# Optimization experiments

Hardware: AMD Instinct MI355X
Metric: run time of the kernel (lower is better)

The kernel has to match this reference:

```python
import jax, jax.numpy as jnp
import numpy as np

V, D, H, B, S, T, N_EXTRA = 32000, 256, 512, 16, 400, 100, 50


def _lstm_cell(x, h, c, Wih, Whh, b):
    g = x @ Wih.T + h @ Whh.T + b
    i, f, gg, o = jnp.split(g, 4, axis=-1)
    c = jax.nn.sigmoid(f) * c + jax.nn.sigmoid(i) * jnp.tanh(gg)
    h = jax.nn.sigmoid(o) * jnp.tanh(c)
    return h, c


def _run_lstm(xs, m, Wih, Whh, b):
    # xs: [S,B,D], m: [S,B,1] validity mask (packed-sequence semantics)
    Bz, Hh = xs.shape[1], Whh.shape[1]
    init = (jnp.zeros((Bz, Hh), xs.dtype), jnp.zeros((Bz, Hh), xs.dtype))
    def step(carry, inp):
        h, c = carry
        x, mm = inp
        hn, cn = _lstm_cell(x, h, c, Wih, Whh, b)
        h = jnp.where(mm, hn, h)
        c = jnp.where(mm, cn, c)
        return (h, c), jnp.where(mm, hn, 0.0)
    (h, c), ys = jax.lax.scan(step, init, (xs, m))
    return ys, h, c


def setup_inputs():
    key = jax.random.key(0)
    ks = jax.random.split(key, 20)
    def gn(k, shape, scale=0.05):
        return jax.random.normal(k, shape, dtype=jnp.float32) * scale
    inp = {}
    inp["source"] = jax.random.randint(ks[0], (B, S), 0, V)
    inp["source_extended"] = jax.random.randint(ks[1], (B, S), 0, V + N_EXTRA)
    inp["source_length"] = jax.random.randint(ks[2], (B,), S // 2, S + 1)
    inp["target"] = jax.random.randint(ks[3], (B, T), 0, V)
    inp["emb"] = gn(ks[4], (V, D), 0.1)
    inp["enc_Wih_f"] = gn(ks[5], (4 * H, D))
    inp["enc_Whh_f"] = gn(ks[6], (4 * H, H))
    inp["enc_b_f"] = jnp.zeros((4 * H,), jnp.float32)
    inp["enc_Wih_b"] = gn(ks[7], (4 * H, D))
    inp["enc_Whh_b"] = gn(ks[8], (4 * H, H))
    inp["enc_b_b"] = jnp.zeros((4 * H,), jnp.float32)
    inp["Wproj"] = gn(ks[9], (H, 2 * H))
    inp["bproj"] = jnp.zeros((H,), jnp.float32)
    inp["W2h"] = gn(ks[10], (H, 2 * H))
    inp["b2h"] = jnp.zeros((H,), jnp.float32)
    inp["W2c"] = gn(ks[11], (H, 2 * H))
    inp["b2c"] = jnp.zeros((H,), jnp.float32)
    inp["Wo1"] = gn(ks[12], (H, 2 * H))
    inp["bo1"] = jnp.zeros((H,), jnp.float32)
    inp["Wo2"] = gn(ks[13], (D, H))
    inp["dec_Wih"] = gn(ks[14], (4 * H, 2 * D))
    inp["dec_Whh"] = gn(ks[15], (4 * H, H))
    inp["dec_b"] = jnp.zeros((4 * H,), jnp.float32)
    inp["Wpgen"] = gn(ks[16], (1, 2 * H + 2 * D))
    inp["bpgen"] = jnp.zeros((1,), jnp.float32)
    return inp


def reference(source, source_extended, source_length, target, emb,
              enc_Wih_f, enc_Whh_f, enc_b_f, enc_Wih_b, enc_Whh_b, enc_b_b,
              Wproj, bproj, W2h, b2h, W2c, b2c, Wo1, bo1, Wo2,
              dec_Wih, dec_Whh, dec_b, Wpgen, bpgen):
    mask = jnp.arange(S)[None, :] < source_length[:, None]  # [B,S]
    w_s = emb[source]                                        # [B,S,D]
    xs = jnp.swapaxes(w_s, 0, 1)                             # [S,B,D]
    m = jnp.swapaxes(mask, 0, 1)[:, :, None]                 # [S,B,1]
    # bidirectional LSTM encoder
    ys_f, h_f, c_f = _run_lstm(xs, m, enc_Wih_f, enc_Whh_f, enc_b_f)
    ys_b, h_b, c_b = _run_lstm(xs[::-1], m[::-1], enc_Wih_b, enc_Whh_b, enc_b_b)
    ys_b = ys_b[::-1]
    enc_outs = jnp.swapaxes(jnp.concatenate([ys_f, ys_b], -1), 0, 1)  # [B,S,2H]
    enc_outs = enc_outs @ Wproj.T + bproj                             # [B,S,H]
    dec_h = jnp.concatenate([h_f, h_b], -1) @ W2h.T + b2h             # [B,H]
    dec_c = jnp.concatenate([c_f, c_b], -1) @ W2c.T + b2c             # [B,H]
    lens = source_length[:, None].astype(enc_outs.dtype)
    seq_mean = (enc_outs * mask[..., None]).sum(1) / lens             # [B,H]
    def out_proj(x):
        return jnp.tanh(x @ Wo1.T + bo1) @ Wo2.T
    dec_out0 = out_proj(jnp.concatenate([dec_h, seq_mean], -1))       # [B,D]
    neg = jnp.finfo(enc_outs.dtype).min
    extra = jnp.zeros((B, N_EXTRA), enc_outs.dtype)
    rows = jnp.arange(B)[:, None]
    w_t = jnp.swapaxes(emb[target], 0, 1)                             # [T,B,D]
    def step(carry, x_t):
        dec_out, h, c = carry
        x = jnp.concatenate([x_t, dec_out], -1)                       # [B,2D]
        h, c = _lstm_cell(x, h, c, dec_Wih, dec_Whh, dec_b)
        scores = jnp.einsum('bh,bsh->bs', h, enc_outs)
        attn = jax.nn.softmax(jnp.where(mask, scores, neg), axis=-1)  # point_dist
        context = jnp.einsum('bs,bsh->bh', attn, enc_outs)
        p_gen = jax.nn.sigmoid(jnp.concatenate([context, h, x], -1) @ Wpgen.T + bpgen)  # [B,1]
        dec_out = out_proj(jnp.concatenate([h, context], -1))         # [B,D]
        logit = dec_out @ emb.T                                       # [B,V]
        vocab_dist = jnp.concatenate([p_gen * jax.nn.softmax(logit, axis=-1), extra], -1)
        final = vocab_dist.at[rows, source_extended].add((1.0 - p_gen) * attn) + 1e-20
        return (dec_out, h, c), jnp.log(final)
    _, logits = jax.lax.scan(step, (dec_out0, dec_h, dec_c), w_t)
    return logits  # [T,B,V+N_EXTRA]
```

## Files before the change

kernel.cpp:

```cpp
#include <hip/hip_runtime.h>

#define V_SZ 32000
#define D_SZ 256
#define H_SZ 512
#define B_SZ 16
#define S_SZ 400
#define T_SZ 100
#define G4   2048
#define VX   32050
#define LINE 32

typedef unsigned short ushort_t;
typedef __attribute__((ext_vector_type(8))) __bf16 bf16x8;
typedef __attribute__((ext_vector_type(8))) unsigned short ushort8_t;
typedef __attribute__((ext_vector_type(4))) float f32x4;

__device__ __forceinline__ ushort_t f2bf(float x) {
  union { float f; unsigned u; } v; v.f = x;
  unsigned r = v.u + 0x7fffu + ((v.u >> 16) & 1u);
  return (ushort_t)(r >> 16);
}
__device__ __forceinline__ float bf2f(ushort_t x) {
  union { unsigned u; float f; } v; v.u = ((unsigned)x) << 16; return v.f;
}
__device__ __forceinline__ float bfu2f(unsigned x) {
  union { unsigned u; float f; } v; v.u = x << 16; return v.f;
}
__device__ __forceinline__ float sigf(float x) { return 1.0f / (1.0f + __expf(-x)); }
__device__ __forceinline__ float tanh_f(float x) {
  float e = __expf(2.0f * x);
  return 1.0f - 2.0f / (e + 1.0f);
}
__device__ __forceinline__ float dot4(f32x4 a, f32x4 b) {
  return a.x * b.x + a.y * b.y + a.z * b.z + a.w * b.w;
}
__device__ __forceinline__ void stg(float* p, float v) {
  __hip_atomic_store(p, v, __ATOMIC_RELAXED, __HIP_MEMORY_SCOPE_AGENT);
}
__device__ __forceinline__ void stg_u32(unsigned* p, unsigned v) {
  __hip_atomic_store(p, v, __ATOMIC_RELAXED, __HIP_MEMORY_SCOPE_AGENT);
}
__device__ __forceinline__ unsigned pollu(const unsigned* p) {
  return __hip_atomic_load(p, __ATOMIC_RELAXED, __HIP_MEMORY_SCOPE_AGENT);
}
__device__ __forceinline__ unsigned ld_sc0(const unsigned* p) {
  unsigned v;
  asm volatile("global_load_dword %0, %1, off sc0\n\ts_waitcnt vmcnt(0)"
               : "=&v"(v) : "v"(p) : "memory");
  return v;
}
__device__ __forceinline__ int xcc_id() {
  unsigned v;
  asm volatile("s_getreg_b32 %0, hwreg(HW_REG_XCC_ID)" : "=s"(v));
  return (int)(v & 0xf);
}

__device__ __forceinline__ void slot_barrier(unsigned* slots, int myslot, int nslots,
                                             unsigned pc) {
  asm volatile("s_waitcnt vmcnt(0)" ::: "memory");
  __syncthreads();
  if (threadIdx.x == 0)
    __hip_atomic_store(&slots[myslot * LINE], pc, __ATOMIC_RELAXED, __HIP_MEMORY_SCOPE_AGENT);
  if (threadIdx.x < 64) {
    const int i0 = threadIdx.x, i1 = threadIdx.x + 64;
    for (;;) {
      unsigned v0 = pc, v1 = pc;
      if (i0 < nslots)
        v0 = __hip_atomic_load(&slots[i0 * LINE], __ATOMIC_RELAXED, __HIP_MEMORY_SCOPE_AGENT);
      if (i1 < nslots)
        v1 = __hip_atomic_load(&slots[i1 * LINE], __ATOMIC_RELAXED, __HIP_MEMORY_SCOPE_AGENT);
      if (__all((v0 >= pc) & (v1 >= pc))) break;
      __builtin_amdgcn_s_sleep(1);
    }
  }
  __syncthreads();
}

__global__ __launch_bounds__(256) void cvt_kernel(const float* in, ushort_t* outp, int n) {
  int i = blockIdx.x * 256 + threadIdx.x;
  int stride = gridDim.x * 256;
  for (; i < n; i += stride) outp[i] = f2bf(in[i]);
}

__global__ __launch_bounds__(256) void cvt_strided_kernel(const float* in, ushort_t* outp) {
  int gid = blockIdx.x * 256 + threadIdx.x;
  int r = gid >> 8, d = gid & 255;
  outp[gid] = f2bf(in[(size_t)r * 512 + d]);
}

__global__ __launch_bounds__(256) void cvt_wo2t_kernel(const float* wo2, ushort_t* outp) {
  int gid = blockIdx.x * 256 + threadIdx.x;
  int h = gid >> 8, d = gid & 255;
  outp[gid] = f2bf(wo2[(size_t)d * 512 + h]);
}

__global__ __launch_bounds__(256) void wfused_kernel(const float* dwih, const float* wo2,
                                                     float* wf) {
  __shared__ float xr_s[256];
  int r = blockIdx.x;
  xr_s[threadIdx.x] = dwih[(size_t)r * 512 + 256 + threadIdx.x];
  __syncthreads();
  float a0 = 0, a1 = 0;
  for (int d = 0; d < 256; ++d) {
    float x = xr_s[d];
    a0 += x * wo2[(size_t)d * 512 + threadIdx.x];
    a1 += x * wo2[(size_t)d * 512 + threadIdx.x + 256];
  }
  wf[(size_t)r * 512 + threadIdx.x] = a0;
  wf[(size_t)r * 512 + threadIdx.x + 256] = a1;
}

__global__ __launch_bounds__(256) void wfp_kernel(const float* wpgen, const float* wo2,
                                                  float* wfp) {
  int h = blockIdx.x * 256 + threadIdx.x;
  float a = 0;
  for (int d = 0; d < 256; ++d) a += wpgen[1280 + d] * wo2[(size_t)d * 512 + h];
  wfp[h] = a;
}

__global__ __launch_bounds__(256) void pack_whh_kernel(const float* whh_f, const float* whh_b,
                                                       ushort_t* outp) {
  int gid = blockIdx.x * 256 + threadIdx.x;
  int col = gid & 511;
  int p_g = gid >> 9;
  int dir = p_g >> 11, p = p_g & 2047;
  int ub = p >> 6, g = (p >> 4) & 3, u = p & 15;
  const float* src = dir ? whh_b : whh_f;
  outp[gid] = f2bf(src[(size_t)(g * 512 + ub * 16 + u) * 512 + col]);
// ... 94 lines not shown
      int m = m0 + kh * 4 + i;
      int b = m & 15, si = m >> 4;
      enc_outs[((size_t)b * S_SZ + si) * H_SZ + n] = acc[s][i] + bv;
    }
  }
}

__global__ __launch_bounds__(256) void gemm_e2(const ushort_t* emb_bf, const ushort_t* wo2t_bf,
                                               ushort_t* e2) {
  int wave = threadIdx.x >> 6;
  int m0 = blockIdx.y * 16;
  int n0 = blockIdx.x * 256 + wave * 64;
  f32x4 acc[4] = {};
  mfma_16x64(emb_bf, wo2t_bf, 256, m0, n0, acc);
  int lane = threadIdx.x & 63, lr = lane & 15, kh = lane >> 4;
#pragma unroll
  for (int s = 0; s < 4; ++s) {
    int n = n0 + s * 16 + lr;
#pragma unroll
    for (int i = 0; i < 4; ++i) {
      int m = m0 + kh * 4 + i;
      e2[(size_t)m * 512 + n] = f2bf(acc[s][i]);
    }
  }
}

__global__ __launch_bounds__(256) void gemm_logits(const ushort_t* tmp_bf, const ushort_t* e2_bf,
                                                   float* out) {
  int wave = threadIdx.x >> 6;
  int m0 = blockIdx.x * 16;
  int n0 = blockIdx.y * 256 + wave * 64;
  f32x4 acc[4] = {};
  mfma_16x64(tmp_bf, e2_bf, 512, m0, n0, acc);
  int lane = threadIdx.x & 63, lr = lane & 15, kh = lane >> 4;
#pragma unroll
  for (int s = 0; s < 4; ++s) {
    int n = n0 + s * 16 + lr;
#pragma unroll
    for (int i = 0; i < 4; ++i) {
      int m = m0 + kh * 4 + i;
      out[(size_t)m * VX + n] = acc[s][i];
    }
  }
}

__global__ __launch_bounds__(256, 1) void enc_kernel(const float* gx_f, const float* gx_b,
                                                     const ushort_t* whh_pk, const int* src_len,
                                                     unsigned* hb_f, unsigned* hb_b,
                                                     unsigned* hbM_f, unsigned* hbM_b,
                                                     unsigned* ys_cat_u32, float* h_final,
                                                     float* c_final, unsigned* ctrs) {
  __shared__ float big_s[25600];
  __shared__ int role_s;
  __shared__ int ok_s;
  float* gates_s = big_s;
  const int tid = threadIdx.x;
  if (tid == 0) {
    int xcc = xcc_id();
    int r = -1;
    if (xcc == 0) {
      unsigned i = atomicAdd(&ctrs[12288], 1u);
      if (i < 32u) r = (int)i;
    } else if (xcc == 1) {
      unsigned i = atomicAdd(&ctrs[12320], 1u);
      if (i < 32u) r = 32 + (int)i;
    }
    role_s = r;
  }
  __syncthreads();
  const int role = role_s;
  if (role < 0) return;
  const int dir = role >> 5, ub = role & 31, j0 = ub * 16;
  const int g = tid >> 6, lane = tid & 63, lr = lane & 15, kh = lane >> 4;
  const float* gx = dir ? gx_b : gx_f;
  unsigned* hb = dir ? hb_b : hb_f;
  unsigned* hbM = dir ? hbM_b : hbM_f;
  unsigned* tl = ctrs + dir * 1024;
  unsigned* tm = ctrs + 2048 + dir * 1024;
  const ushort_t* wrow =
      whh_pk + (size_t)(((dir * 32 + ub) * 4 + g) * 16 + lr) * 512 + kh * 8;
  const int bc = tid >> 4, uc = tid & 15;
  const int len_b = src_len[bc];
  float c_reg = 0.0f, h_reg = 0.0f;
  bool slow = false;

  int maxlen;
  {
    int v = src_len[lane & 15];
    v = max(v, __shfl_xor(v, 1));
    v = max(v, __shfl_xor(v, 2));
    v = max(v, __shfl_xor(v, 4));
    v = max(v, __shfl_xor(v, 8));
    maxlen = v;
  }
  for (int i = tid; i < (S_SZ - maxlen) * 128; i += 256) {
    int s = maxlen + (i >> 7);
    int r2 = i & 127;
    int bb = r2 >> 3, k = r2 & 7;
    ys_cat_u32[(size_t)(s * 16 + bb) * 512 + dir * 256 + (j0 >> 1) + k] = 0u;
  }

  float gxa[4];
  {
    const int s0 = dir ? (maxlen - 1) : 0;
    const float* g0 = gx + (size_t)s0 * (16 * 2048) + g * 512 + j0 + lr;
#pragma unroll
    for (int i = 0; i < 4; ++i) gxa[i] = g0[(size_t)(kh * 4 + i) * 2048];
  }

  for (int t = 0; t < maxlen; ++t) {
    const int s_pos = dir ? (maxlen - 1 - t) : t;
    float gxn[4] = {0.f, 0.f, 0.f, 0.f};
    if (t + 1 < maxlen) {
      const int sn = dir ? (maxlen - 2 - t) : (t + 1);
      const float* gn = gx + (size_t)sn * (16 * 2048) + g * 512 + j0 + lr;
#pragma unroll
      for (int i = 0; i < 4; ++i) gxn[i] = gn[(size_t)(kh * 4 + i) * 2048];
    }
    const unsigned* hsrcbuf = hb;
    if (t > 0) {
      if (tid < 64) {
        int ok = 0;
        if (!slow) {
          for (int it = 0; it < 2000; ++it) {
            unsigned v = (unsigned)t;
            if (lane < 32) v = ld_sc0(&tl[lane * 32]);
            if (__all((int)(v >= (unsigned)t))) { ok = 1; break; }
            __builtin_amdgcn_s_sleep(1);
          }
        }
        if (!ok) {
          for (;;) {
            unsigned v = (unsigned)t;
            if (lane < 32) v = pollu(&tm[lane * 32]);
            if (__all((int)(v >= (unsigned)t))) break;
            __builtin_amdgcn_s_sleep(1);
          }
        }
        if (tid == 0) ok_s = ok;
      }
      __syncthreads();
      if (!ok_s) slow = true;
      hsrcbuf = ok_s ? hb : hbM;
    }
    f32x4 acc = {0.f, 0.f, 0.f, 0.f};
    const ushort_t* ap = (const ushort_t*)(hsrcbuf + (size_t)t * 4096) + lr * 512 + kh * 8;
#pragma unroll
    for (int k0 = 0; k0 < 512; k0 += 32)
      acc = __builtin_amdgcn_mfma_f32_16x16x32_bf16(*(const bf16x8*)(ap + k0),
                                                    *(const bf16x8*)(wrow + k0), acc, 0, 0, 0);
#pragma unroll
    for (int i = 0; i < 4; ++i)
      gates_s[(g * 16 + lr) * 17 + kh * 4 + i] = acc[i] + gxa[i];
    __syncthreads();
    float gi = gates_s[uc * 17 + bc];
    float gf = gates_s[(16 + uc) * 17 + bc];
    float gg = gates_s[(32 + uc) * 17 + bc];
    float go = gates_s[(48 + uc) * 17 + bc];
    bool msk = s_pos < len_b;
    float cn = sigf(gf) * c_reg + sigf(gi) * tanh_f(gg);
    float hn = sigf(go) * tanh_f(cn);
    float hout = msk ? hn : h_reg;
    if (msk) c_reg = cn;
    h_reg = hout;
    unsigned hbits = (unsigned)f2bf(hout);
    unsigned hpart = __shfl_xor(hbits, 1);
    unsigned ybits = msk ? (unsigned)f2bf(hn) : 0u;
    unsigned ypart = __shfl_xor(ybits, 1);
    if ((uc & 1) == 0) {
      unsigned wv2 = hbits | (hpart << 16);
      size_t ix = (size_t)(t + 1) * 4096 + bc * 256 + ((j0 + uc) >> 1);
      hb[ix] = wv2;
      stg_u32(&hbM[ix], wv2);
      ys_cat_u32[(size_t)(s_pos * 16 + bc) * 512 + dir * 256 + ((j0 + uc) >> 1)] =
          ybits | (ypart << 16);
    }
    if (t == maxlen - 1) {
      h_final[dir * 8192 + bc * 512 + j0 + uc] = hout;
      c_final[dir * 8192 + bc * 512 + j0 + uc] = c_reg;
    }
    asm volatile("s_waitcnt vmcnt(0)" ::: "memory");
    __syncthreads();
    if (tid == 0) {
      tl[ub * 32] = (unsigned)(t + 1);
      stg_u32(&tm[ub * 32], (unsigned)(t + 1));
    }
#pragma unroll
    for (int i = 0; i < 4; ++i) gxa[i] = gxn[i];
  }
}

__global__ __launch_bounds__(256) void seqmean_kernel(const float* enc_outs, const int* src_len,
                                                      float* seq_mean) {
  int b = blockIdx.x >> 1;
  int j = (blockIdx.x & 1) * 256 + threadIdx.x;
  int L = src_len[b];
  float a = 0;
  for (int s = 0; s < L; ++s) a += enc_outs[((size_t)b * S_SZ + s) * H_SZ + j];
  seq_mean[b * 512 + j] = a / (float)L;
}

__global__ __launch_bounds__(256) void init_state_kernel(const float* h_final, const float* c_final,
                                                         const float* w2h, const float* b2h,
                                                         const float* w2c, const float* b2c,
                                                         unsigned* h_u32, float* c_init) {
  int gid = blockIdx.x * 256 + threadIdx.x;
  int half = gid >> 13;
  int idx = gid & 8191;
  int b = idx >> 9, j = idx & 511;
  const float* src = half ? c_final : h_final;
  const float* w = (half ? w2c : w2h) + (size_t)j * 1024;
  float acc = (half ? b2c : b2h)[j];
  const f32x4* s0 = (const f32x4*)(src + b * 512);
  const f32x4* s1 = (const f32x4*)(src + 8192 + b * 512);
  const f32x4* w0 = (const f32x4*)w;
  const f32x4* w1 = w0 + 128;
  float a = 0;
  for (int k = 0; k < 128; ++k) a += dot4(s0[k], w0[k]);
  for (int k = 0; k < 128; ++k) a += dot4(s1[k], w1[k]);
  acc += a;
  if (half) {
    c_init[idx] = acc;
  } else {
    unsigned bits = (unsigned)f2bf(acc);
    unsigned pb2 = __shfl_xor(bits, 1);
    if ((j & 1) == 0) h_u32[b * 256 + (j >> 1)] = bits | (pb2 << 16);
  }
}

__global__ __launch_bounds__(256) void tmp0_kernel(const unsigned* h0_u32, const float* seq_mean,
                                                   const float* wo1, const float* bo1,
                                                   unsigned* tmp_u32) {
  int gid = blockIdx.x * 256 + threadIdx.x;
  int b = gid >> 9, j = gid & 511;
  const f32x4* x1 = (const f32x4*)(seq_mean + b * 512);
  const f32x4* w0 = (const f32x4*)(wo1 + (size_t)j * 1024);
  const f32x4* w1 = w0 + 128;
  float a = bo1[j];
  float p = 0;
  const ushort_t* h0 = (const ushort_t*)(h0_u32) + b * 512;
  for (int k = 0; k < 128; ++k) {
    f32x4 hv = {bf2f(h0[k * 4]), bf2f(h0[k * 4 + 1]), bf2f(h0[k * 4 + 2]), bf2f(h0[k * 4 + 3])};
    p += dot4(hv, w0[k]);
  }
  for (int k = 0; k < 128; ++k) p += dot4(x1[k], w1[k]);
  float tv = tanh_f(a + p);
  unsigned bits = (unsigned)f2bf(tv);
  unsigned pb2 = __shfl_xor(bits, 1);
  if ((j & 1) == 0) tmp_u32[b * 256 + (j >> 1)] = bits | (pb2 << 16);
}

__global__ __launch_bounds__(256) void dec_kernel(
    const ushort_t* xt_bf, const int* src_len, const ushort_t* wdec_pk,
    const float* wpgen, const float* bpgen, const float* wfp, const ushort_t* wo1_bf,
    const float* bo1, const float* enc_outs, const float* gxT, unsigned* h_u32,
    const float* c_init, unsigned* tmp_u32, float* ctx_part, float* z_part, float* zinv,
    float* pgen_o, float* pexp, unsigned* ctrs) {
  __shared__ ushort_t ec_s[50 * 512];
  __shared__ float part_s[4 * 16 * 17];
  __shared__ f32x4 smem4[272];
  __shared__ float red_s[8];
  __shared__ float p_s[64];
  float* sm = (float*)smem4;
  unsigned* gslots = ctrs + 4096;

  const int blk = blockIdx.x, tid = threadIdx.x;
  const int w = tid >> 6, lane = tid & 63, lr = lane & 15, kh = lane >> 4;
  const int j0 = blk * 4;
  const ushort_t* wrow = wdec_pk + (size_t)(blk * 16 + lr) * 1024 + w * 256 + kh * 8;
  const int b_c = (tid >> 2) & 15, u_c = tid & 3;
  float c_reg = (tid < 64) ? c_init[b_c * 512 + j0 + u_c] : 0.0f;
  const int b_pb = blk >> 3, ch = blk & 7, s0c = ch * 50;
  const int len_pb = src_len[b_pb];
  const int nc = ch;
  unsigned* grslots = ctrs + 8192 + b_pb * 256;
  unsigned gpc = 0;

  {
    const f32x4* ebase = (const f32x4*)(enc_outs + ((size_t)b_pb * S_SZ + s0c) * H_SZ);
    unsigned* dst = (unsigned*)ec_s;
    for (int i = tid; i < 6400; i += 256) {
      f32x4 v = ebase[i];
      dst[2 * i] = (unsigned)f2bf(v.x) | ((unsigned)f2bf(v.y) << 16);
      dst[2 * i + 1] = (unsigned)f2bf(v.z) | ((unsigned)f2bf(v.w) << 16);
    }
  }

  float gxa[4] = {0.f, 0.f, 0.f, 0.f};
  if (tid < 64) {
#pragma unroll
    for (int g2 = 0; g2 < 4; ++g2)
      gxa[g2] = gxT[((size_t)(g2 * 512 + j0 + u_c)) * 16 + b_c];
  }

  for (int t = 0; t < T_SZ; ++t) {
    {
      f32x4 acc = {0.f, 0.f, 0.f, 0.f};
      const unsigned* asrc = (w < 2) ? (h_u32 + (size_t)t * 4096) : (tmp_u32 + (size_t)t * 4096);
      const ushort_t* ap = (const ushort_t*)asrc + lr * 512 + (w & 1) * 256 + kh * 8;
#pragma unroll
      for (int k0 = 0; k0 < 256; k0 += 32)
        acc = __builtin_amdgcn_mfma_f32_16x16x32_bf16(*(const bf16x8*)(ap + k0),
                                                      *(const bf16x8*)(wrow + k0), acc, 0, 0, 0);
#pragma unroll
      for (int i = 0; i < 4; ++i) part_s[(w * 16 + lr) * 17 + kh * 4 + i] = acc[i];
      __syncthreads();
      if (tid < 64) {
        float gt[4];
#pragma unroll
        for (int g2 = 0; g2 < 4; ++g2) {
          int p = g2 * 4 + u_c;
          float a = gxa[g2];
#pragma unroll
          for (int w2 = 0; w2 < 4; ++w2) a += part_s[(w2 * 16 + p) * 17 + b_c];
          gt[g2] = a;
        }
        float cn = sigf(gt[1]) * c_reg + sigf(gt[0]) * tanh_f(gt[2]);
        c_reg = cn;
        float hn = sigf(gt[3]) * tanh_f(cn);
        unsigned bits = (unsigned)f2bf(hn);
        unsigned pb2 = __shfl_xor(bits, 1);
        if ((u_c & 1) == 0)
          stg_u32(&h_u32[(size_t)(t + 1) * 4096 + b_c * 256 + ((j0 + u_c) >> 1)],
                  bits | (pb2 << 16));
      }
    }
    slot_barrier(gslots, blk, 128, ++gpc);
    {
      if (tid < 64 && t + 1 < T_SZ) {
#pragma unroll
        for (int g2 = 0; g2 < 4; ++g2)
          gxa[g2] = gxT[((size_t)(t + 1) * G4 + g2 * 512 + j0 + u_c) * 16 + b_c];
      }
      if (tid < 128) {
        unsigned v0 = h_u32[(size_t)(t + 1) * 4096 + b_pb * 256 + tid * 2];
        unsigned v1 = h_u32[(size_t)(t + 1) * 4096 + b_pb * 256 + tid * 2 + 1];
        f32x4 hv = {bfu2f(v0 & 0xffffu), bfu2f(v0 >> 16), bfu2f(v1 & 0xffffu), bfu2f(v1 >> 16)};
        ((f32x4*)sm)[tid] = hv;
      }
      __syncthreads();
      int st = tid >> 2, kq = tid & 3;
      if (st < 50) {
        const ushort8_t* er = (const ushort8_t*)(ec_s + st * 512) + kq * 16;
        const f32x4* hr = (const f32x4*)sm + kq * 32;
        float sc = 0;
#pragma unroll 4
        for (int k = 0; k < 16; ++k) {
          ushort8_t w8 = er[k];
          f32x4 w0 = {bf2f(w8[0]), bf2f(w8[1]), bf2f(w8[2]), bf2f(w8[3])};
          f32x4 w1 = {bf2f(w8[4]), bf2f(w8[5]), bf2f(w8[6]), bf2f(w8[7])};
          sc += dot4(hr[2 * k], w0) + dot4(hr[2 * k + 1], w1);
        }
        sc += __shfl_xor(sc, 1);
        sc += __shfl_xor(sc, 2);
        if (kq == 0) {
          int s_abs = s0c + st;
          float p = (s_abs < len_pb) ? __expf(sc) : 0.0f;
          p_s[st] = p;
          pexp[((size_t)t * 16 + b_pb) * S_SZ + s_abs] = p;
        }
      }
      __syncthreads();
      if (tid == 0) {
        float z = 0;
        for (int s = 0; s < 50; ++s) z += p_s[s];
        stg(&z_part[((size_t)t * 16 + b_pb) * 8 + ch], z);
      }
      float a0 = 0, a1 = 0;
      for (int s = 0; s < 50; ++s) {
        float p = p_s[s];
        a0 += p * bf2f(ec_s[s * 512 + tid]);
        a1 += p * bf2f(ec_s[s * 512 + tid + 256]);
      }
      float* cp = ctx_part + (((size_t)t * 16 + b_pb) * 8 + ch) * 512;
      stg(&cp[tid], a0);
      stg(&cp[tid + 256], a1);
    }
    slot_barrier(grslots, ch, 8, (unsigned)(t + 1));
    {
      float* h_s = sm;
      float* ctx_s = sm + 512;
      const float* zp = z_part + ((size_t)t * 16 + b_pb) * 8;
      float z = 0;
#pragma unroll
      for (int c2 = 0; c2 < 8; ++c2) z += zp[c2];
      float inv = 1.0f / z;
      const float* cpb = ctx_part + ((size_t)t * 16 + b_pb) * 8 * 512;
      float c0 = 0, c1 = 0;
#pragma unroll
      for (int c2 = 0; c2 < 8; ++c2) {
        c0 += cpb[c2 * 512 + tid];
        c1 += cpb[c2 * 512 + tid + 256];
      }
      ctx_s[tid] = c0 * inv;
      ctx_s[tid + 256] = c1 * inv;
      __syncthreads();
      const ushort_t* tmpp = (const ushort_t*)(tmp_u32 + (size_t)t * 4096) + b_pb * 512;
      float tp0 = bf2f(tmpp[tid]);
      float tp1 = bf2f(tmpp[tid + 256]);
      float xe = bf2f(xt_bf[((size_t)t * 16 + b_pb) * 256 + tid]);
      float pg = wpgen[tid] * ctx_s[tid] + wpgen[tid + 256] * ctx_s[tid + 256] +
                 wpgen[512 + tid] * h_s[tid] + wpgen[512 + tid + 256] * h_s[tid + 256] +
                 wpgen[1024 + tid] * xe + wfp[tid] * tp0 + wfp[tid + 256] * tp1;
#pragma unroll
      for (int o = 32; o; o >>= 1) pg += __shfl_xor(pg, o);
      if (lane == 0) red_s[w] = pg;
      __syncthreads();
      if (nc == 0 && tid == 0) {
        pgen_o[t * 16 + b_pb] = sigf(red_s[0] + red_s[1] + red_s[2] + red_s[3] + bpgen[0]);
        zinv[t * 16 + b_pb] = inv;
      }
      int nidx = tid >> 2, kq = tid & 3;
      int n = nc * 64 + nidx;
      const ushort8_t* wrp = (const ushort8_t*)(wo1_bf + (size_t)n * 1024) + kq * 32;
      const f32x4* xr2 =
          (kq < 2) ? ((const f32x4*)h_s + kq * 64) : ((const f32x4*)ctx_s + (kq - 2) * 64);
      float a = 0;
#pragma unroll 4
      for (int k = 0; k < 32; ++k) {
        ushort8_t w8 = wrp[k];
        f32x4 w0 = {bf2f(w8[0]), bf2f(w8[1]), bf2f(w8[2]), bf2f(w8[3])};
        f32x4 w1 = {bf2f(w8[4]), bf2f(w8[5]), bf2f(w8[6]), bf2f(w8[7])};
        a += dot4(xr2[2 * k], w0) + dot4(xr2[2 * k + 1], w1);
      }
      a += __shfl_xor(a, 1);
      a += __shfl_xor(a, 2);
      float tv = tanh_f(a + bo1[n]);
      unsigned bits = (unsigned)f2bf(tv);
      unsigned pbits = __shfl_xor(bits, 4);
      if (kq == 0 && (nidx & 1) == 0)
        stg_u32(&tmp_u32[(size_t)(t + 1) * 4096 + b_pb * 256 + ((nc * 64 + nidx) >> 1)],
                bits | (pbits << 16));
    }
    if (t + 1 < T_SZ) slot_barrier(gslots, blk, 128, ++gpc);
  }
}

__global__ __launch_bounds__(1024) void finalize_kernel(float* out, const float* pexp,
                                                        const float* zinv, const float* pgen_i,
                                                        const int* src_ext) {
  __shared__ float scat[VX];
  __shared__ float red[64];
  const int row = blockIdx.x;
  const int b = row & 15;
  const int tid = threadIdx.x;
  for (int i = tid; i < VX; i += 1024) scat[i] = 0.0f;
  __syncthreads();
  const float pg = pgen_i[row];
  const float inv = zinv[row];
  if (tid < S_SZ) {
    float v = (1.0f - pg) * pexp[(size_t)row * S_SZ + tid] * inv;
    int col = src_ext[b * S_SZ + tid];
    atomicAdd(&scat[col], v);
  }
  float* orow = out + (size_t)row * VX;
  float l[32];
  float mx = -3.4e38f;
#pragma unroll
  for (int i2 = 0; i2 < 32; ++i2) {
    int col = tid + (i2 << 10);
    l[i2] = (col < V_SZ) ? orow[col] : -3.4e38f;
    mx = fmaxf(mx, l[i2]);
  }
#pragma unroll
  for (int o = 32; o; o >>= 1) mx = fmaxf(mx, __shfl_xor(mx, o));
  if ((tid & 63) == 0) red[16 + (tid >> 6)] = mx;
  __syncthreads();
  if (tid == 0) {
    float m2 = red[16];
    for (int w = 1; w < 16; ++w) m2 = fmaxf(m2, red[16 + w]);
    red[0] = m2;
  }
  __syncthreads();
  const float gmx = red[0];
  float se = 0.0f;
#pragma unroll
  for (int i2 = 0; i2 < 32; ++i2) {
    int col = tid + (i2 << 10);
    if (col < V_SZ) {
      l[i2] = __expf(l[i2] - gmx);
      se += l[i2];
    }
  }
#pragma unroll
  for (int o = 32; o; o >>= 1) se += __shfl_xor(se, o);
  if ((tid & 63) == 0) red[32 + (tid >> 6)] = se;
  __syncthreads();
// ... 1 lines not shown
    float s2 = 0;
    for (int w = 0; w < 16; ++w) s2 += red[32 + w];
    red[1] = s2;
  }
  __syncthreads();
  const float scale = pg / red[1];
#pragma unroll
  for (int i2 = 0; i2 < 32; ++i2) {
    int col = tid + (i2 << 10);
    if (col < VX) {
      float base = (col < V_SZ) ? l[i2] * scale : 0.0f;
      orow[col] = __logf(base + scat[col] + 1e-20f);
    }
  }
}

extern "C" void kernel_launch(void* const* d_in, const int* in_sizes, int n_in, void* d_out,
                              int out_size, void* d_ws, size_t ws_size, hipStream_t stream) {
  (void)in_sizes; (void)n_in; (void)out_size; (void)ws_size;
  const int* source = (const int*)d_in[0];
  const int* source_ext = (const int*)d_in[1];
  const int* source_len = (const int*)d_in[2];
  const int* target = (const int*)d_in[3];
  const float* emb = (const float*)d_in[4];
  const float* wih_f = (const float*)d_in[5];
  const float* whh_f = (const float*)d_in[6];
  const float* b_f = (const float*)d_in[7];
  const float* wih_b = (const float*)d_in[8];
  const float* whh_b = (const float*)d_in[9];
  const float* b_b = (const float*)d_in[10];
  const float* wproj = (const float*)d_in[11];
  const float* bproj = (const float*)d_in[12];
  const float* w2h = (const float*)d_in[13];
  const float* b2h = (const float*)d_in[14];
  const float* w2c = (const float*)d_in[15];
  const float* b2c = (const float*)d_in[16];
  const float* wo1 = (const float*)d_in[17];
  const float* bo1 = (const float*)d_in[18];
  const float* wo2 = (const float*)d_in[19];
  const float* dwih = (const float*)d_in[20];
  const float* dwhh = (const float*)d_in[21];
  const float* dbias = (const float*)d_in[22];
  const float* wpgen = (const float*)d_in[23];
  const float* bpgen = (const float*)d_in[24];
  float* out = (float*)d_out;

  size_t off = 0;
  char* wsb = (char*)d_ws;
  auto alloc = [&](size_t bytes) -> void* {
    void* p = wsb + off;
    off += (bytes + 255) & ~(size_t)255;
    return p;
  };
  unsigned* ctrs = (unsigned*)alloc(64 * 1024);
  ushort_t* emb_bf = (ushort_t*)alloc((size_t)V_SZ * D_SZ * 2);
  ushort_t* wihf_bf = (ushort_t*)alloc((size_t)G4 * D_SZ * 2);
  ushort_t* wihb_bf = (ushort_t*)alloc((size_t)G4 * D_SZ * 2);
  ushort_t* wihd_bf = (ushort_t*)alloc((size_t)G4 * D_SZ * 2);
  ushort_t* wproj_bf = (ushort_t*)alloc((size_t)H_SZ * 2 * H_SZ * 2);
  ushort_t* wo2t_bf = (ushort_t*)alloc((size_t)H_SZ * D_SZ * 2);
  ushort_t* wo1_bf = (ushort_t*)alloc((size_t)H_SZ * 1024 * 2);
  float* wfused = (float*)alloc((size_t)G4 * H_SZ * 4);
  float* wfp = (float*)alloc(512 * 4);
  ushort_t* whh_pk = (ushort_t*)alloc((size_t)2 * G4 * H_SZ * 2);
  ushort_t* wdec_pk = (ushort_t*)alloc((size_t)G4 * 1024 * 2);
  ushort_t* xs_bf = (ushort_t*)alloc((size_t)S_SZ * B_SZ * D_SZ * 2);
  ushort_t* xt_bf = (ushort_t*)alloc((size_t)T_SZ * B_SZ * D_SZ * 2);
  float* gx_f = (float*)alloc((size_t)S_SZ * B_SZ * G4 * 4);
  float* gx_b = (float*)alloc((size_t)S_SZ * B_SZ * G4 * 4);
  unsigned* hb_f = (unsigned*)alloc((size_t)(S_SZ + 1) * 4096 * 4);
  unsigned* hb_b = (unsigned*)alloc((size_t)(S_SZ + 1) * 4096 * 4);
  unsigned* hbM_f = (unsigned*)alloc((size_t)(S_SZ + 1) * 4096 * 4);
  unsigned* hbM_b = (unsigned*)alloc((size_t)(S_SZ + 1) * 4096 * 4);
  unsigned* ys_cat_u32 = (unsigned*)alloc((size_t)S_SZ * B_SZ * 512 * 4);
  float* h_final = (float*)alloc((size_t)2 * B_SZ * H_SZ * 4);
  float* c_final = (float*)alloc((size_t)2 * B_SZ * H_SZ * 4);
  float* enc_outs = (float*)alloc((size_t)B_SZ * S_SZ * H_SZ * 4);
  float* seq_mean = (float*)alloc((size_t)B_SZ * H_SZ * 4);
  unsigned* h_u32 = (unsigned*)alloc((size_t)(T_SZ + 1) * 4096 * 4);
  float* c_init = (float*)alloc((size_t)B_SZ * H_SZ * 4);
  unsigned* tmp_u32 = (unsigned*)alloc((size_t)(T_SZ + 1) * 4096 * 4);
  float* z_part = (float*)alloc((size_t)T_SZ * B_SZ * 8 * 4);
  float* zinv = (float*)alloc((size_t)T_SZ * B_SZ * 4);
  float* pgen_b = (float*)alloc((size_t)T_SZ * B_SZ * 4);
  float* pexp = (float*)alloc((size_t)T_SZ * B_SZ * S_SZ * 4);
  ushort_t* e2_bf = (ushort_t*)gx_f;
  float* gx_dec = gx_b;
  float* ctx_part = gx_b + (size_t)3276800;
  float* gxT = gx_b + (size_t)9830400;

  hipMemsetAsync(ctrs, 0, 64 * 1024, stream);
  hipMemsetAsync(hb_f, 0, 4096 * 4, stream);
  hipMemsetAsync(hb_b, 0, 4096 * 4, stream);
  hipMemsetAsync(hbM_f, 0, 4096 * 4, stream);
  hipMemsetAsync(hbM_b, 0, 4096 * 4, stream);

  cvt_kernel<<<2048, 256, 0, stream>>>(emb, emb_bf, V_SZ * D_SZ);
  cvt_kernel<<<2048, 256, 0, stream>>>(wih_f, wihf_bf, G4 * D_SZ);
  cvt_kernel<<<2048, 256, 0, stream>>>(wih_b, wihb_bf, G4 * D_SZ);
  cvt_kernel<<<2048, 256, 0, stream>>>(wproj, wproj_bf, H_SZ * 2 * H_SZ);
  cvt_kernel<<<2048, 256, 0, stream>>>(wo1, wo1_bf, H_SZ * 1024);
  cvt_strided_kernel<<<2048, 256, 0, stream>>>(dwih, wihd_bf);
  cvt_wo2t_kernel<<<512, 256, 0, stream>>>(wo2, wo2t_bf);
  wfused_kernel<<<2048, 256, 0, stream>>>(dwih, wo2, wfused);
  wfp_kernel<<<2, 256, 0, stream>>>(wpgen, wo2, wfp);
  pack_whh_kernel<<<8192, 256, 0, stream>>>(whh_f, whh_b, whh_pk);
  pack_wdec_kernel<<<8192, 256, 0, stream>>>(dwhh, wfused, wdec_pk);
  gather_src_kernel<<<800, 256, 0, stream>>>(emb_bf, source, xs_bf);
  gather_tgt_kernel<<<200, 256, 0, stream>>>(emb_bf, target, xt_bf);
  gemm_abt_bias<<<dim3(8, 400), 256, 0, stream>>>(xs_bf, wihf_bf, b_f, gx_f, 256);
  gemm_abt_bias<<<dim3(8, 400), 256, 0, stream>>>(xs_bf, wihb_bf, b_b, gx_b, 256);
  enc_kernel<<<256, 256, 0, stream>>>(gx_f, gx_b, whh_pk, source_len, hb_f, hb_b, hbM_f, hbM_b,
                                      ys_cat_u32, h_final, c_final, ctrs);
  gemm_encout<<<dim3(2, 400), 256, 0, stream>>>((const ushort_t*)ys_cat_u32, wproj_bf, bproj,
                                                enc_outs);
  seqmean_kernel<<<32, 256, 0, stream>>>(enc_outs, source_len, seq_mean);
  init_state_kernel<<<64, 256, 0, stream>>>(h_final, c_final, w2h, b2h, w2c, b2c, h_u32, c_init);
  tmp0_kernel<<<32, 256, 0, stream>>>(h_u32, seq_mean, wo1, bo1, tmp_u32);
  gemm_abt_bias<<<dim3(8, 100), 256, 0, stream>>>(xt_bf, wihd_bf, dbias, gx_dec, 256);
  gxT_kernel<<<dim3(8, 100), 256, 0, stream>>>(gx_dec, gxT);
  gemm_e2<<<dim3(2, 2000), 256, 0, stream>>>(emb_bf, wo2t_bf, e2_bf);
  dec_kernel<<<128, 256, 0, stream>>>(xt_bf, source_len, wdec_pk, wpgen, bpgen, wfp, wo1_bf, bo1,
                                      enc_outs, gxT, h_u32, c_init, tmp_u32, ctx_part, z_part,
                                      zinv, pgen_b, pexp, ctrs);
  gemm_logits<<<dim3(100, 125), 256, 0, stream>>>((const ushort_t*)(tmp_u32 + 4096), e2_bf, out);
  finalize_kernel<<<1600, 1024, 0, stream>>>(out, pexp, zinv, pgen_b, source_ext);
}
```

Before: 5.045 ms.

## Replace counter barriers with sentinel-valued data polling in encoder and decoder

Drops the per-step counter and slot barriers in the persistent encoder and decoder kernels. Consumers now poll the produced data itself (h state, ctx partials, z partials, tmp), which is pre-filled with a 0xFFFFFFFF sentinel, until no sentinel word remains. The recurrent weights are also hoisted into registers once per kernel. This is meant to cut the barrier round-trip latency on every sequential step. In exchange it adds large memsets of the state and partial buffers and more register pressure, and it relies on real data never equalling the sentinel and on each multi-dword value being seen as a whole.

```diff
diff --git a/kernel.cpp b/kernel.cpp
--- a/kernel.cpp
+++ b/kernel.cpp
@@ -8,12 +8,15 @@
 #define T_SZ 100
 #define G4   2048
 #define VX   32050
-#define LINE 32
+#define SENTU 0xFFFFFFFFu
 
 typedef unsigned short ushort_t;
 typedef __attribute__((ext_vector_type(8))) __bf16 bf16x8;
 typedef __attribute__((ext_vector_type(8))) unsigned short ushort8_t;
 typedef __attribute__((ext_vector_type(4))) float f32x4;
+typedef __attribute__((ext_vector_type(4))) unsigned u32x4;
+
+union UU { u32x4 q; bf16x8 v; };
 
 __device__ __forceinline__ ushort_t f2bf(float x) {
   union { float f; unsigned u; } v; v.f = x;
@@ -26,6 +29,9 @@
 __device__ __forceinline__ float bfu2f(unsigned x) {
   union { unsigned u; float f; } v; v.u = x << 16; return v.f;
 }
+__device__ __forceinline__ float u2f(unsigned x) {
+  union { unsigned u; float f; } v; v.u = x; return v.f;
+}
 __device__ __forceinline__ float sigf(float x) { return 1.0f / (1.0f + __expf(-x)); }
 __device__ __forceinline__ float tanh_f(float x) {
   float e = __expf(2.0f * x);
@@ -40,40 +46,19 @@
 __device__ __forceinline__ void stg_u32(unsigned* p, unsigned v) {
   __hip_atomic_store(p, v, __ATOMIC_RELAXED, __HIP_MEMORY_SCOPE_AGENT);
 }
-__device__ __forceinline__ unsigned pollu(const unsigned* p) {
-  return __hip_atomic_load(p, __ATOMIC_RELAXED, __HIP_MEMORY_SCOPE_AGENT);
-}
-__device__ __forceinline__ unsigned ld_sc0(const unsigned* p) {
-  unsigned v;
-  asm volatile("global_load_dword %0, %1, off sc0\n\ts_waitcnt vmcnt(0)"
-               : "=&v"(v) : "v"(p) : "memory");
-  return v;
-}
 __device__ __forceinline__ int xcc_id() {
   unsigned v;
   asm volatile("s_getreg_b32 %0, hwreg(HW_REG_XCC_ID)" : "=s"(v));
   return (int)(v & 0xf);
 }
-
-__device__ __forceinline__ void slot_barrier(unsigned* slots, int myslot, int nslots,
-                                             unsigned pc) {
-  asm volatile("s_waitcnt vmcnt(0)" ::: "memory");
-  __syncthreads();
-  if (threadIdx.x == 0)
-    __hip_atomic_store(&slots[myslot * LINE], pc, __ATOMIC_RELAXED, __HIP_MEMORY_SCOPE_AGENT);
-  if (threadIdx.x < 64) {
-    const int i0 = threadIdx.x, i1 = threadIdx.x + 64;
-    for (;;) {
-      unsigned v0 = pc, v1 = pc;
-      if (i0 < nslots)
-        v0 = __hip_atomic_load(&slots[i0 * LINE], __ATOMIC_RELAXED, __HIP_MEMORY_SCOPE_AGENT);
-      if (i1 < nslots)
-        v1 = __hip_atomic_load(&slots[i1 * LINE], __ATOMIC_RELAXED, __HIP_MEMORY_SCOPE_AGENT);
-      if (__all((v0 >= pc) & (v1 >= pc))) break;
-      __builtin_amdgcn_s_sleep(1);
-    }
-  }
-  __syncthreads();
+__device__ __forceinline__ unsigned okq(u32x4 c) {
+  return (unsigned)((c.x != SENTU) & (c.y != SENTU) & (c.z != SENTU) & (c.w != SENTU));
+}
+__device__ __forceinline__ u32x4 ld1_ic(const unsigned* p) {
+  u32x4 v;
+  asm volatile("global_load_dwordx4 %0, %1, off sc0 sc1\n\ts_waitcnt vmcnt(0)"
+               : "=&v"(v) : "v"(p) : "memory");
+  return v;
 }
 
 __global__ __launch_bounds__(256) void cvt_kernel(const float* in, ushort_t* outp, int n) {
@@ -274,17 +259,16 @@
                                                      float* c_final, unsigned* ctrs) {
   __shared__ float big_s[25600];
   __shared__ int role_s;
-  __shared__ int ok_s;
   float* gates_s = big_s;
   const int tid = threadIdx.x;
   if (tid == 0) {
     int xcc = xcc_id();
     int r = -1;
     if (xcc == 0) {
-      unsigned i = atomicAdd(&ctrs[12288], 1u);
+      unsigned i = atomicAdd(&ctrs[0], 1u);
       if (i < 32u) r = (int)i;
     } else if (xcc == 1) {
-      unsigned i = atomicAdd(&ctrs[12320], 1u);
+      unsigned i = atomicAdd(&ctrs[32], 1u);
       if (i < 32u) r = 32 + (int)i;
     }
     role_s = r;
@@ -297,14 +281,16 @@
   const float* gx = dir ? gx_b : gx_f;
   unsigned* hb = dir ? hb_b : hb_f;
   unsigned* hbM = dir ? hbM_b : hbM_f;
-  unsigned* tl = ctrs + dir * 1024;
-  unsigned* tm = ctrs + 2048 + dir * 1024;
   const ushort_t* wrow =
       whh_pk + (size_t)(((dir * 32 + ub) * 4 + g) * 16 + lr) * 512 + kh * 8;
   const int bc = tid >> 4, uc = tid & 15;
   const int len_b = src_len[bc];
   float c_reg = 0.0f, h_reg = 0.0f;
   bool slow = false;
+
+  bf16x8 wv[16];
+#pragma unroll
+  for (int k = 0; k < 16; ++k) wv[k] = *(const bf16x8*)(wrow + k * 32);
 
   int maxlen;
   {
@@ -339,38 +325,86 @@
 #pragma unroll
       for (int i = 0; i < 4; ++i) gxn[i] = gn[(size_t)(kh * 4 + i) * 2048];
     }
-    const unsigned* hsrcbuf = hb;
-    if (t > 0) {
-      if (tid < 64) {
-        int ok = 0;
-        if (!slow) {
-          for (int it = 0; it < 2000; ++it) {
-            unsigned v = (unsigned)t;
-            if (lane < 32) v = ld_sc0(&tl[lane * 32]);
-            if (__all((int)(v >= (unsigned)t))) { ok = 1; break; }
-            __builtin_amdgcn_s_sleep(1);
-          }
+    UU hv[16];
+    if (t == 0) {
+#pragma unroll
+      for (int k = 0; k < 16; ++k) hv[k].q = (u32x4){0u, 0u, 0u, 0u};
+    } else {
+      const unsigned* hpL = hb + (size_t)t * 4096 + lr * 256 + kh * 4;
+      const unsigned* hpM = hbM + (size_t)t * 4096 + lr * 256 + kh * 4;
+      bool done = false;
+      if (!slow) {
+        for (int r3 = 0; r3 < 1500 && !done; ++r3) {
+          asm volatile(
+              "global_load_dwordx4 %0, %16, off sc0\n\t"
+              "global_load_dwordx4 %1, %16, off offset:64 sc0\n\t"
+              "global_load_dwordx4 %2, %16, off offset:128 sc0\n\t"
+              "global_load_dwordx4 %3, %16, off offset:192 sc0\n\t"
+              "global_load_dwordx4 %4, %16, off offset:256 sc0\n\t"
+              "global_load_dwordx4 %5, %16, off offset:320 sc0\n\t"
+              "global_load_dwordx4 %6, %16, off offset:384 sc0\n\t"
+              "global_load_dwordx4 %7, %16, off offset:448 sc0\n\t"
+              "global_load_dwordx4 %8, %16, off offset:512 sc0\n\t"
+              "global_load_dwordx4 %9, %16, off offset:576 sc0\n\t"
+              "global_load_dwordx4 %10, %16, off offset:640 sc0\n\t"
+              "global_load_dwordx4 %11, %16, off offset:704 sc0\n\t"
+              "global_load_dwordx4 %12, %16, off offset:768 sc0\n\t"
+              "global_load_dwordx4 %13, %16, off offset:832 sc0\n\t"
+              "global_load_dwordx4 %14, %16, off offset:896 sc0\n\t"
+              "global_load_dwordx4 %15, %16, off offset:960 sc0\n\t"
+              "s_waitcnt vmcnt(0)"
+              : "=&v"(hv[0].q), "=&v"(hv[1].q), "=&v"(hv[2].q), "=&v"(hv[3].q),
+                "=&v"(hv[4].q), "=&v"(hv[5].q), "=&v"(hv[6].q), "=&v"(hv[7].q),
+                "=&v"(hv[8].q), "=&v"(hv[9].q), "=&v"(hv[10].q), "=&v"(hv[11].q),
+                "=&v"(hv[12].q), "=&v"(hv[13].q), "=&v"(hv[14].q), "=&v"(hv[15].q)
+              : "v"(hpL)
+              : "memory");
+          unsigned ok = 1;
+#pragma unroll
+          for (int k = 0; k < 16; ++k) ok &= okq(hv[k].q);
+          if (__all((int)ok)) done = true;
+          else __builtin_amdgcn_s_sleep(1);
         }
-        if (!ok) {
-          for (;;) {
-            unsigned v = (unsigned)t;
-            if (lane < 32) v = pollu(&tm[lane * 32]);
-            if (__all((int)(v >= (unsigned)t))) break;
-            __builtin_amdgcn_s_sleep(1);
-          }
+        if (!done) slow = true;
+      }
+      if (!done) {
+        for (;;) {
+          asm volatile(
+              "global_load_dwordx4 %0, %16, off sc0 sc1\n\t"
+              "global_load_dwordx4 %1, %16, off offset:64 sc0 sc1\n\t"
+              "global_load_dwordx4 %2, %16, off offset:128 sc0 sc1\n\t"
+              "global_load_dwordx4 %3, %16, off offset:192 sc0 sc1\n\t"
+              "global_load_dwordx4 %4, %16, off offset:256 sc0 sc1\n\t"
+              "global_load_dwordx4 %5, %16, off offset:320 sc0 sc1\n\t"
+              "global_load_dwordx4 %6, %16, off offset:384 sc0 sc1\n\t"
+              "global_load_dwordx4 %7, %16, off offset:448 sc0 sc1\n\t"
+              "global_load_dwordx4 %8, %16, off offset:512 sc0 sc1\n\t"
+              "global_load_dwordx4 %9, %16, off offset:576 sc0 sc1\n\t"
+              "global_load_dwordx4 %10, %16, off offset:640 sc0 sc1\n\t"
+              "global_load_dwordx4 %11, %16, off offset:704 sc0 sc1\n\t"
+              "global_load_dwordx4 %12, %16, off offset:768 sc0 sc1\n\t"
+              "global_load_dwordx4 %13, %16, off offset:832 sc0 sc1\n\t"
+              "global_load_dwordx4 %14, %16, off offset:896 sc0 sc1\n\t"
+              "global_load_dwordx4 %15, %16, off offset:960 sc0 sc1\n\t"
+              "s_waitcnt vmcnt(0)"
+              : "=&v"(hv[0].q), "=&v"(hv[1].q), "=&v"(hv[2].q), "=&v"(hv[3].q),
+                "=&v"(hv[4].q), "=&v"(hv[5].q), "=&v"(hv[6].q), "=&v"(hv[7].q),
+                "=&v"(hv[8].q), "=&v"(hv[9].q), "=&v"(hv[10].q), "=&v"(hv[11].q),
+                "=&v"(hv[12].q), "=&v"(hv[13].q), "=&v"(hv[14].q), "=&v"(hv[15].q)
+              : "v"(hpM)
+              : "memory");
+          unsigned ok = 1;
+#pragma unroll
+          for (int k = 0; k < 16; ++k) ok &= okq(hv[k].q);
+          if (__all((int)ok)) break;
+          __builtin_amdgcn_s_sleep(1);
         }
-        if (tid == 0) ok_s = ok;
-      }
-      __syncthreads();
-      if (!ok_s) slow = true;
-      hsrcbuf = ok_s ? hb : hbM;
+      }
     }
     f32x4 acc = {0.f, 0.f, 0.f, 0.f};
-    const ushort_t* ap = (const ushort_t*)(hsrcbuf + (size_t)t * 4096) + lr * 512 + kh * 8;
-#pragma unroll
-    for (int k0 = 0; k0 < 512; k0 += 32)
-      acc = __builtin_amdgcn_mfma_f32_16x16x32_bf16(*(const bf16x8*)(ap + k0),
-                                                    *(const bf16x8*)(wrow + k0), acc, 0, 0, 0);
+#pragma unroll
+    for (int k = 0; k < 16; ++k)
+      acc = __builtin_amdgcn_mfma_f32_16x16x32_bf16(hv[k].v, wv[k], acc, 0, 0, 0);
 #pragma unroll
     for (int i = 0; i < 4; ++i)
       gates_s[(g * 16 + lr) * 17 + kh * 4 + i] = acc[i] + gxa[i];
@@ -401,12 +435,7 @@
       h_final[dir * 8192 + bc * 512 + j0 + uc] = hout;
       c_final[dir * 8192 + bc * 512 + j0 + uc] = c_reg;
     }
-    asm volatile("s_waitcnt vmcnt(0)" ::: "memory");
     __syncthreads();
-    if (tid == 0) {
-      tl[ub * 32] = (unsigned)(t + 1);
-      stg_u32(&tm[ub * 32], (unsigned)(t + 1));
-    }
 #pragma unroll
     for (int i = 0; i < 4; ++i) gxa[i] = gxn[i];
   }
@@ -477,14 +506,13 @@
     const float* wpgen, const float* bpgen, const float* wfp, const ushort_t* wo1_bf,
     const float* bo1, const float* enc_outs, const float* gxT, unsigned* h_u32,
     const float* c_init, unsigned* tmp_u32, float* ctx_part, float* z_part, float* zinv,
-    float* pgen_o, float* pexp, unsigned* ctrs) {
+    float* pgen_o, float* pexp) {
   __shared__ ushort_t ec_s[50 * 512];
   __shared__ float part_s[4 * 16 * 17];
   __shared__ f32x4 smem4[272];
   __shared__ float red_s[8];
   __shared__ float p_s[64];
   float* sm = (float*)smem4;
-  unsigned* gslots = ctrs + 4096;
 
   const int blk = blockIdx.x, tid = threadIdx.x;
   const int w = tid >> 6, lane = tid & 63, lr = lane & 15, kh = lane >> 4;
@@ -495,8 +523,10 @@
   const int b_pb = blk >> 3, ch = blk & 7, s0c = ch * 50;
   const int len_pb = src_len[b_pb];
   const int nc = ch;
-  unsigned* grslots = ctrs + 8192 + b_pb * 256;
-  unsigned gpc = 0;
+
+  bf16x8 wv[8];
+#pragma unroll
+  for (int k = 0; k < 8; ++k) wv[k] = *(const bf16x8*)(wrow + k * 32);
 
   {
     const f32x4* ebase = (const f32x4*)(enc_outs + ((size_t)b_pb * S_SZ + s0c) * H_SZ);
@@ -517,13 +547,34 @@
 
   for (int t = 0; t < T_SZ; ++t) {
     {
+      const unsigned* asrc = (w < 2) ? (h_u32 + (size_t)t * 4096) : (tmp_u32 + (size_t)t * 4096);
+      const unsigned* hp = asrc + lr * 256 + (w & 1) * 128 + kh * 4;
+      UU hv[8];
+      for (;;) {
+        asm volatile(
+            "global_load_dwordx4 %0, %8, off sc0 sc1\n\t"
+            "global_load_dwordx4 %1, %8, off offset:64 sc0 sc1\n\t"
+            "global_load_dwordx4 %2, %8, off offset:128 sc0 sc1\n\t"
+            "global_load_dwordx4 %3, %8, off offset:192 sc0 sc1\n\t"
+            "global_load_dwordx4 %4, %8, off offset:256 sc0 sc1\n\t"
+            "global_load_dwordx4 %5, %8, off offset:320 sc0 sc1\n\t"
+            "global_load_dwordx4 %6, %8, off offset:384 sc0 sc1\n\t"
+            "global_load_dwordx4 %7, %8, off offset:448 sc0 sc1\n\t"
+            "s_waitcnt vmcnt(0)"
+            : "=&v"(hv[0].q), "=&v"(hv[1].q), "=&v"(hv[2].q), "=&v"(hv[3].q),
+              "=&v"(hv[4].q), "=&v"(hv[5].q), "=&v"(hv[6].q), "=&v"(hv[7].q)
+            : "v"(hp)
+            : "memory");
+        unsigned ok = 1;
+#pragma unroll
+        for (int k = 0; k < 8; ++k) ok &= okq(hv[k].q);
+        if (__all((int)ok)) break;
+        __builtin_amdgcn_s_sleep(1);
+      }
       f32x4 acc = {0.f, 0.f, 0.f, 0.f};
-      const unsigned* asrc = (w < 2) ? (h_u32 + (size_t)t * 4096) : (tmp_u32 + (size_t)t * 4096);
-      const ushort_t* ap = (const ushort_t*)asrc + lr * 512 + (w & 1) * 256 + kh * 8;
-#pragma unroll
-      for (int k0 = 0; k0 < 256; k0 += 32)
-        acc = __builtin_amdgcn_mfma_f32_16x16x32_bf16(*(const bf16x8*)(ap + k0),
-                                                      *(const bf16x8*)(wrow + k0), acc, 0, 0, 0);
+#pragma unroll
+      for (int k = 0; k < 8; ++k)
+        acc = __builtin_amdgcn_mfma_f32_16x16x32_bf16(hv[k].v, wv[k], acc, 0, 0, 0);
 #pragma unroll
       for (int i = 0; i < 4; ++i) part_s[(w * 16 + lr) * 17 + kh * 4 + i] = acc[i];
       __syncthreads();
@@ -546,19 +597,28 @@
           stg_u32(&h_u32[(size_t)(t + 1) * 4096 + b_c * 256 + ((j0 + u_c) >> 1)],
                   bits | (pb2 << 16));
       }
-    }
-    slot_barrier(gslots, blk, 128, ++gpc);
+      __syncthreads();
+    }
     {
       if (tid < 64 && t + 1 < T_SZ) {
 #pragma unroll
         for (int g2 = 0; g2 < 4; ++g2)
           gxa[g2] = gxT[((size_t)(t + 1) * G4 + g2 * 512 + j0 + u_c) * 16 + b_c];
       }
-      if (tid < 128) {
-        unsigned v0 = h_u32[(size_t)(t + 1) * 4096 + b_pb * 256 + tid * 2];
-        unsigned v1 = h_u32[(size_t)(t + 1) * 4096 + b_pb * 256 + tid * 2 + 1];
-        f32x4 hv = {bfu2f(v0 & 0xffffu), bfu2f(v0 >> 16), bfu2f(v1 & 0xffffu), bfu2f(v1 >> 16)};
-        ((f32x4*)sm)[tid] = hv;
+      if (tid < 64) {
+        const unsigned* hp = h_u32 + (size_t)(t + 1) * 4096 + b_pb * 256 + tid * 4;
+        u32x4 v;
+        for (;;) {
+          v = ld1_ic(hp);
+          if (__all((int)okq(v))) break;
+          __builtin_amdgcn_s_sleep(1);
+        }
+        f32x4 h0 = {bfu2f(v.x & 0xffffu), bfu2f(v.x >> 16), bfu2f(v.y & 0xffffu),
+                    bfu2f(v.y >> 16)};
+        f32x4 h1 = {bfu2f(v.z & 0xffffu), bfu2f(v.z >> 16), bfu2f(v.w & 0xffffu),
+                    bfu2f(v.w >> 16)};
+        ((f32x4*)sm)[tid * 2] = h0;
+        ((f32x4*)sm)[tid * 2 + 1] = h1;
       }
       __syncthreads();
       int st = tid >> 2, kq = tid & 3;
@@ -594,32 +654,53 @@
         a0 += p * bf2f(ec_s[s * 512 + tid]);
         a1 += p * bf2f(ec_s[s * 512 + tid + 256]);
       }
-      float* cp = ctx_part + (((size_t)t * 16 + b_pb) * 8 + ch) * 512;
-      stg(&cp[tid], a0);
-      stg(&cp[tid + 256], a1);
-    }
-    slot_barrier(grslots, ch, 8, (unsigned)(t + 1));
+      float* cpb2 = ctx_part + ((size_t)t * 16 + b_pb) * 4096;
+      stg(&cpb2[tid * 8 + ch], a0);
+      stg(&cpb2[(tid + 256) * 8 + ch], a1);
+    }
     {
       float* h_s = sm;
       float* ctx_s = sm + 512;
-      const float* zp = z_part + ((size_t)t * 16 + b_pb) * 8;
-      float z = 0;
-#pragma unroll
-      for (int c2 = 0; c2 < 8; ++c2) z += zp[c2];
+      const unsigned* pa = (const unsigned*)(ctx_part + ((size_t)t * 16 + b_pb) * 4096 +
+                                             (size_t)tid * 8);
+      const unsigned* pb2 = (const unsigned*)(ctx_part + ((size_t)t * 16 + b_pb) * 4096 +
+                                              (size_t)(tid + 256) * 8);
+      const unsigned* pz = (const unsigned*)(z_part + ((size_t)t * 16 + b_pb) * 8);
+      const unsigned* pt = tmp_u32 + (size_t)t * 4096 + b_pb * 256 + (tid >> 1);
+      u32x4 ca0, ca1, cb0, cb1, zq0, zq1;
+      unsigned t0v, t1v;
+      for (;;) {
+        asm volatile(
+            "global_load_dwordx4 %0, %8, off sc0 sc1\n\t"
+            "global_load_dwordx4 %1, %8, off offset:16 sc0 sc1\n\t"
+            "global_load_dwordx4 %2, %9, off sc0 sc1\n\t"
+            "global_load_dwordx4 %3, %9, off offset:16 sc0 sc1\n\t"
+            "global_load_dwordx4 %4, %10, off sc0 sc1\n\t"
+            "global_load_dwordx4 %5, %10, off offset:16 sc0 sc1\n\t"
+            "global_load_dword %6, %11, off sc0 sc1\n\t"
+            "global_load_dword %7, %11, off offset:512 sc0 sc1\n\t"
+            "s_waitcnt vmcnt(0)"
+            : "=&v"(ca0), "=&v"(ca1), "=&v"(cb0), "=&v"(cb1), "=&v"(zq0), "=&v"(zq1),
+              "=&v"(t0v), "=&v"(t1v)
+            : "v"(pa), "v"(pb2), "v"(pz), "v"(pt)
+            : "memory");
+        unsigned ok = okq(ca0) & okq(ca1) & okq(cb0) & okq(cb1) & okq(zq0) & okq(zq1) &
+                      (unsigned)((t0v != SENTU) & (t1v != SENTU));
+        if (__all((int)ok)) break;
+        __builtin_amdgcn_s_sleep(1);
+      }
+      float z = u2f(zq0.x) + u2f(zq0.y) + u2f(zq0.z) + u2f(zq0.w) + u2f(zq1.x) + u2f(zq1.y) +
+                u2f(zq1.z) + u2f(zq1.w);
       float inv = 1.0f / z;
-      const float* cpb = ctx_part + ((size_t)t * 16 + b_pb) * 8 * 512;
-      float c0 = 0, c1 = 0;
-#pragma unroll
-      for (int c2 = 0; c2 < 8; ++c2) {
-        c0 += cpb[c2 * 512 + tid];
-        c1 += cpb[c2 * 512 + tid + 256];
-      }
+      float c0 = u2f(ca0.x) + u2f(ca0.y) + u2f(ca0.z) + u2f(ca0.w) + u2f(ca1.x) + u2f(ca1.y) +
+                 u2f(ca1.z) + u2f(ca1.w);
+      float c1 = u2f(cb0.x) + u2f(cb0.y) + u2f(cb0.z) + u2f(cb0.w) + u2f(cb1.x) + u2f(cb1.y) +
+                 u2f(cb1.z) + u2f(cb1.w);
       ctx_s[tid] = c0 * inv;
       ctx_s[tid + 256] = c1 * inv;
       __syncthreads();
-      const ushort_t* tmpp = (const ushort_t*)(tmp_u32 + (size_t)t * 4096) + b_pb * 512;
-      float tp0 = bf2f(tmpp[tid]);
-      float tp1 = bf2f(tmpp[tid + 256]);
+      float tp0 = bf2f((ushort_t)((tid & 1) ? (t0v >> 16) : (t0v & 0xffffu)));
+      float tp1 = bf2f((ushort_t)((tid & 1) ? (t1v >> 16) : (t1v & 0xffffu)));
       float xe = bf2f(xt_bf[((size_t)t * 16 + b_pb) * 256 + tid]);
       float pg = wpgen[tid] * ctx_s[tid] + wpgen[tid + 256] * ctx_s[tid + 256] +
                  wpgen[512 + tid] * h_s[tid] + wpgen[512 + tid + 256] * h_s[tid + 256] +
@@ -653,8 +734,8 @@
       if (kq == 0 && (nidx & 1) == 0)
         stg_u32(&tmp_u32[(size_t)(t + 1) * 4096 + b_pb * 256 + ((nc * 64 + nidx) >> 1)],
                 bits | (pbits << 16));
-    }
-    if (t + 1 < T_SZ) slot_barrier(gslots, blk, 128, ++gpc);
+      __syncthreads();
+    }
   }
 }
 
@@ -762,7 +843,7 @@
     off += (bytes + 255) & ~(size_t)255;
     return p;
   };
-  unsigned* ctrs = (unsigned*)alloc(64 * 1024);
+  unsigned* ctrs = (unsigned*)alloc(4096);
   ushort_t* emb_bf = (ushort_t*)alloc((size_t)V_SZ * D_SZ * 2);
   ushort_t* wihf_bf = (ushort_t*)alloc((size_t)G4 * D_SZ * 2);
   ushort_t* wihb_bf = (ushort_t*)alloc((size_t)G4 * D_SZ * 2);
@@ -799,11 +880,14 @@
   float* ctx_part = gx_b + (size_t)3276800;
   float* gxT = gx_b + (size_t)9830400;
 
-  hipMemsetAsync(ctrs, 0, 64 * 1024, stream);
-  hipMemsetAsync(hb_f, 0, 4096 * 4, stream);
-  hipMemsetAsync(hb_b, 0, 4096 * 4, stream);
-  hipMemsetAsync(hbM_f, 0, 4096 * 4, stream);
-  hipMemsetAsync(hbM_b, 0, 4096 * 4, stream);
+  hipMemsetAsync(ctrs, 0, 4096, stream);
+  hipMemsetAsync(hb_f, 0xFF, (size_t)(S_SZ + 1) * 4096 * 4, stream);
+  hipMemsetAsync(hb_b, 0xFF, (size_t)(S_SZ + 1) * 4096 * 4, stream);
+  hipMemsetAsync(hbM_f, 0xFF, (size_t)(S_SZ + 1) * 4096 * 4, stream);
+  hipMemsetAsync(hbM_b, 0xFF, (size_t)(S_SZ + 1) * 4096 * 4, stream);
+  hipMemsetAsync(h_u32, 0xFF, (size_t)(T_SZ + 1) * 4096 * 4, stream);
+  hipMemsetAsync(tmp_u32, 0xFF, (size_t)(T_SZ + 1) * 4096 * 4, stream);
+  hipMemsetAsync(z_part, 0xFF, (size_t)T_SZ * B_SZ * 8 * 4, stream);
 
   cvt_kernel<<<2048, 256, 0, stream>>>(emb, emb_bf, V_SZ * D_SZ);
   cvt_kernel<<<2048, 256, 0, stream>>>(wih_f, wihf_bf, G4 * D_SZ);
@@ -830,9 +914,10 @@
   gemm_abt_bias<<<dim3(8, 100), 256, 0, stream>>>(xt_bf, wihd_bf, dbias, gx_dec, 256);
   gxT_kernel<<<dim3(8, 100), 256, 0, stream>>>(gx_dec, gxT);
   gemm_e2<<<dim3(2, 2000), 256, 0, stream>>>(emb_bf, wo2t_bf, e2_bf);
+  hipMemsetAsync(ctx_part, 0xFF, (size_t)T_SZ * B_SZ * 8 * H_SZ * 4, stream);
   dec_kernel<<<128, 256, 0, stream>>>(xt_bf, source_len, wdec_pk, wpgen, bpgen, wfp, wo1_bf, bo1,
                                       enc_outs, gxT, h_u32, c_init, tmp_u32, ctx_part, z_part,
-                                      zinv, pgen_b, pexp, ctrs);
+                                      zinv, pgen_b, pexp);
   gemm_logits<<<dim3(100, 125), 256, 0, stream>>>((const ushort_t*)(tmp_u32 + 4096), e2_bf, out);
   finalize_kernel<<<1600, 1024, 0, stream>>>(out, pexp, zinv, pgen_b, source_ext);
 }
```

Measured after the change: 7.226 ms. +43.2%, slower.
